# Performance work log

Measured on AMD Instinct MI355X. Metric: run time of the kernel, lower is better.

The kernel has to match this reference:

```python
import jax, jax.numpy as jnp
import numpy as np

B, S, D, H = 2, 2048, 1024, 16
DK = D // H

def setup_inputs() -> dict:
    key = jax.random.key(0)
    ks = jax.random.split(key, 12)
    s = 0.02
    inp = {
        'query': jax.random.normal(ks[0], (B, S, D), jnp.float32),
        'key':   jax.random.normal(ks[1], (B, S, D), jnp.float32),
        'value': jax.random.normal(ks[2], (B, S, D), jnp.float32),
        'mask':  jnp.broadcast_to(jnp.tril(jnp.ones((S, S), jnp.int32)), (B, S, S)),
        'wq': jax.random.normal(ks[3], (D, D), jnp.float32) * s,
        'bq': jnp.zeros((D,), jnp.float32),
        'wk': jax.random.normal(ks[4], (D, D), jnp.float32) * s,
        'bk': jnp.zeros((D,), jnp.float32),
        'wv': jax.random.normal(ks[5], (D, D), jnp.float32) * s,
        'bv': jnp.zeros((D,), jnp.float32),
        'wo': jax.random.normal(ks[6], (D, D), jnp.float32) * s,
        'bo': jnp.zeros((D,), jnp.float32),
    }
    return inp

def reference(query, key, value, mask, wq, bq, wk, bk, wv, bv, wo, bo):
    # Linear projections (torch Linear: x @ W.T + b); W stored (out,in)
    Q = query @ wq.T + bq   # (B,Sq,D)
    K = key   @ wk.T + bk   # (B,Sk,D)
    V = value @ wv.T + bv   # (B,Sk,D)
    # split heads -> (B,H,S,DK)
    Q = Q.reshape(B, S, H, DK).transpose(0, 2, 1, 3)
    K = K.reshape(B, S, H, DK).transpose(0, 2, 1, 3)
    V = V.reshape(B, S, H, DK).transpose(0, 2, 1, 3)
    scores = jnp.einsum('bhqd,bhkd->bhqk', Q, K) / jnp.sqrt(jnp.float32(DK))
    scores = jnp.where(mask[:, None, :, :] == 0, -jnp.inf, scores)
    attn = jax.nn.softmax(scores, axis=-1)  # dropout is identity in eval/reference
    context = jnp.einsum('bhqk,bhkd->bhqd', attn, V)
    context = context.transpose(0, 2, 1, 3).reshape(B, S, D)
    return context @ wo.T + bo
```

## Files before the change

### kernel.cpp

```cpp
#include <hip/hip_runtime.h>
#include <hip/hip_bf16.h>


#define B_ 2
#define S_ 2048
#define D_ 1024
#define H_ 16
#define DK_ 64
#define SZX (4096 * 1024)
#define SZW (1024 * 1024)

typedef __attribute__((ext_vector_type(8))) short short8;
typedef __attribute__((ext_vector_type(4))) float f32x4;
typedef __attribute__((ext_vector_type(16))) float f32x16;

using bf16 = __hip_bfloat16;

__device__ __forceinline__ short8 load8(const bf16* p) {
    return *reinterpret_cast<const short8*>(p);
}

__device__ __forceinline__ f32x4 mfma16(short8 a, short8 b, f32x4 c) {
    return __builtin_amdgcn_mfma_f32_16x16x32_bf16(a, b, c, 0, 0, 0);
}

__device__ __forceinline__ f32x16 mfma32(short8 a, short8 b, f32x16 c) {
    return __builtin_amdgcn_mfma_f32_32x32x16_bf16(a, b, c, 0, 0, 0);
}

__device__ __forceinline__ void async16(const bf16* g, bf16* l) {
    __builtin_amdgcn_global_load_lds(
        (const __attribute__((address_space(1))) void*)g,
        (__attribute__((address_space(3))) void*)l, 16, 0, 0);
}

__device__ __forceinline__ short bf16rne(float f) {
    unsigned u = __float_as_uint(f);
    return (short)((u + 0x7FFFu + ((u >> 16) & 1u)) >> 16);
}

struct CvtArgs {
    const float* src[7];
    bf16* dst[7];
};

__global__ __launch_bounds__(256) void cvt_kernel(CvtArgs a) {
    const long long e = ((long long)blockIdx.x * 256 + threadIdx.x) * 8;
    int t; long long off;
    if (e < 3LL * SZX) { t = (int)(e >> 22); off = e & (SZX - 1); }
    else { const long long e2 = e - 3LL * SZX; t = 3 + (int)(e2 >> 20); off = e2 & (SZW - 1); }
    const float4 f0 = *reinterpret_cast<const float4*>(a.src[t] + off);
    const float4 f1 = *reinterpret_cast<const float4*>(a.src[t] + off + 4);
    short8 o;
    o[0] = bf16rne(f0.x); o[1] = bf16rne(f0.y); o[2] = bf16rne(f0.z); o[3] = bf16rne(f0.w);
    o[4] = bf16rne(f1.x); o[5] = bf16rne(f1.y); o[6] = bf16rne(f1.z); o[7] = bf16rne(f1.w);
    *reinterpret_cast<short8*>((short*)a.dst[t] + off) = o;
}

struct ProjArgs {
    const bf16* X[3]; const bf16* W[3]; const float* bias[3]; void* Y[3]; int mode[3];
};

template <int BM>
__global__ __launch_bounds__(256) void proj_kernel(ProjArgs a) {
    constexpr int MSUB = BM / 32;
    constexpr int WM   = MSUB / 2;

    const int z = blockIdx.z;
    const bf16* __restrict__ X = a.X[z];
    const bf16* __restrict__ W = a.W[z];
    const float* __restrict__ bias = a.bias[z];
    const int mode = a.mode[z];

    __shared__ __align__(16) bf16 lA[MSUB * 4 * 512];
    __shared__ __align__(16) bf16 lB[16 * 512];

    const int tid  = threadIdx.x;
    const int wv   = tid >> 6;
    const int lane = tid & 63;
    const int l31  = lane & 31;
    const int khi  = lane >> 5;
    const int m0   = blockIdx.x * BM;
    const int n0   = blockIdx.y * 128;

    const bf16* gA[MSUB];
    #pragma unroll
    for (int s = 0; s < MSUB; ++s) {
        const int fa = wv * MSUB + s;
        gA[s] = X + (size_t)(m0 + (fa >> 2) * 32 + l31) * D_ + (fa & 3) * 16 + khi * 8;
    }
    const bf16* gB = W + (size_t)(n0 + wv * 32 + l31) * D_ + khi * 8;

    f32x16 acc[WM][2] = {};

    #pragma unroll 1
    for (int k0 = 0; k0 < D_; k0 += 64) {
        #pragma unroll
        for (int s = 0; s < MSUB; ++s)
            async16(gA[s] + k0, &lA[(wv * MSUB + s) * 512]);
        #pragma unroll
        for (int s = 0; s < 4; ++s)
            async16(gB + k0 + s * 16, &lB[(wv * 4 + s) * 512]);
        __syncthreads();

        #pragma unroll
        for (int kk = 0; kk < 4; ++kk) {
            short8 af[WM], bfr[2];
            #pragma unroll
            for (int mi = 0; mi < WM; ++mi)
                af[mi] = load8(&lA[(((wv & 1) * WM + mi) * 4 + kk) * 512 + lane * 8]);
            #pragma unroll
            for (int ni = 0; ni < 2; ++ni)
                bfr[ni] = load8(&lB[(((wv >> 1) * 2 + ni) * 4 + kk) * 512 + lane * 8]);
            #pragma unroll
            for (int mi = 0; mi < WM; ++mi)
                #pragma unroll
                for (int ni = 0; ni < 2; ++ni)
                    acc[mi][ni] = mfma32(af[mi], bfr[ni], acc[mi][ni]);
        }
        __syncthreads();
    }

    #pragma unroll
    for (int ni = 0; ni < 2; ++ni) {
        const int col = n0 + (wv >> 1) * 64 + ni * 32 + l31;
        const float bv = bias[col];
        const int h = col >> 6, d = col & 63;
        #pragma unroll
        for (int mi = 0; mi < WM; ++mi) {
            const int rb = m0 + ((wv & 1) * WM + mi) * 32 + 4 * khi;
            #pragma unroll
            for (int reg = 0; reg < 16; ++reg) {
                const int m = rb + (reg & 3) + 8 * (reg >> 2);
                const float val = acc[mi][ni][reg] + bv;
                if (mode == 3) {
                    ((float*)a.Y[z])[(size_t)m * D_ + col] = val;
                } else {
                    bf16* Y = (bf16*)a.Y[z];
                    const bf16 o = __float2bfloat16(val);
                    const int b  = m >> 11;
                    const int s  = m & (S_ - 1);
                    const int bh = b * H_ + h;
                    if (mode == 2) Y[((size_t)bh * DK_ + d) * S_ + s] = o;
                    else           Y[((size_t)bh * S_ + s) * DK_ + d] = o;
                }
            }
        }
    }
}

__global__ __launch_bounds__(256) void attn_kernel(
    const bf16* __restrict__ Qb, const bf16* __restrict__ Kb,
    const bf16* __restrict__ Vt, bf16* __restrict__ ctx)
{
    __shared__ __align__(16) bf16 Kt[64 * 64];
    __shared__ __align__(16) bf16 Vl[64 * 64];
    __shared__ __align__(16) bf16 lds_p[4][16][72];

    const int tid  = threadIdx.x;
    const int wv   = tid >> 6;
    const int lane = tid & 63;
    const int quad = lane >> 4;
    const int l16  = lane & 15;

    const int bx = blockIdx.x;
    const int bh = (bx & 7) * 4 + ((bx >> 3) & 3);
    const int m  = 31 - (bx >> 5);
    const int q0 = m * 64;
    const int qr = q0 + wv * 16;

    const bf16* Qh = Qb + (size_t)bh * (S_ * DK_);
    const bf16* Kh = Kb + (size_t)bh * (S_ * DK_);
    const bf16* Vh = Vt + (size_t)bh * (DK_ * S_);

    const float c = 0.18033688011112042f;
    const short8 ones = {16256, 16256, 16256, 16256, 16256, 16256, 16256, 16256};

    const int srow  = wv * 8 + (lane >> 3);
    const int sunit = (lane & 7) ^ ((lane >> 3) & 7);

    const short8 qa0 = load8(Qh + (qr + l16) * DK_ + quad * 8);
    const short8 qa1 = load8(Qh + (qr + l16) * DK_ + 32 + quad * 8);

    f32x4 cacc[4] = {};
    f32x4 lsum = {};

    for (int jt = 0; jt <= m; ++jt) {
        const int j0 = jt * 64;

        #pragma unroll
        for (int cc = 0; cc < 2; ++cc) {
            const int r = cc * 32 + srow;
            async16(Kh + (size_t)(j0 + r) * DK_ + sunit * 8, &Kt[(cc * 32 + wv * 8) * 64]);
            async16(Vh + (size_t)r * S_ + j0 + sunit * 8,    &Vl[(cc * 32 + wv * 8) * 64]);
        }
        __syncthreads();

        short8 kb[4][2], vb[4][2];
        #pragma unroll
        for (int t = 0; t < 4; ++t)
            #pragma unroll
            for (int kh = 0; kh < 2; ++kh) {
                const int u = ((kh * 4 + quad) ^ (l16 & 7)) * 8;
                kb[t][kh] = load8(&Kt[(t * 16 + l16) * 64 + u]);
                vb[t][kh] = load8(&Vl[(t * 16 + l16) * 64 + u]);
            }

        f32x4 s[4];
        #pragma unroll
        for (int t = 0; t < 4; ++t) {
            f32x4 zz = {};
            zz = mfma16(qa0, kb[t][0], zz);
            s[t] = mfma16(qa1, kb[t][1], zz);
        }

        if (jt < m) {
            #pragma unroll
            for (int r = 0; r < 4; ++r)
                #pragma unroll
                for (int t = 0; t < 4; ++t)
                    lds_p[wv][quad * 4 + r][t * 16 + l16] =
                        __float2bfloat16(exp2f(c * s[t][r]));
        } else {
            #pragma unroll
            for (int r = 0; r < 4; ++r) {
                const int row = qr + quad * 4 + r;
                #pragma unroll
                for (int t = 0; t < 4; ++t) {
                    const float p = (j0 + t * 16 + l16 <= row) ? exp2f(c * s[t][r]) : 0.f;
                    lds_p[wv][quad * 4 + r][t * 16 + l16] = __float2bfloat16(p);
                }
            }
        }

        asm volatile("s_waitcnt lgkmcnt(0)" ::: "memory");
        const short8 pa0 = load8(&lds_p[wv][l16][quad * 8]);
        const short8 pa1 = load8(&lds_p[wv][l16][32 + quad * 8]);

        #pragma unroll
        for (int dt = 0; dt < 4; ++dt) {
            cacc[dt] = mfma16(pa0, vb[dt][0], cacc[dt]);
            cacc[dt] = mfma16(pa1, vb[dt][1], cacc[dt]);
        }
        lsum = mfma16(pa0, ones, lsum);
        lsum = mfma16(pa1, ones, lsum);

        __syncthreads();
    }

    const int bb = bh >> 4, hh = bh & 15;
    #pragma unroll
    for (int r = 0; r < 4; ++r) {
        const float inv = 1.0f / lsum[r];
        const int row = qr + quad * 4 + r;
        bf16* orow = ctx + (size_t)(bb * S_ + row) * D_ + hh * DK_;
        #pragma unroll
        for (int dt = 0; dt < 4; ++dt)
            orow[dt * 16 + l16] = __float2bfloat16(cacc[dt][r] * inv);
    }
}

extern "C" void kernel_launch(void* const* d_in, const int* in_sizes, int n_in,
                              void* d_out, int out_size, void* d_ws, size_t ws_size,
                              hipStream_t stream) {
    (void)in_sizes; (void)n_in; (void)out_size; (void)ws_size;
    const float* q  = (const float*)d_in[0];
    const float* k  = (const float*)d_in[1];
    const float* v  = (const float*)d_in[2];
    const float* wq = (const float*)d_in[4];
    const float* bq = (const float*)d_in[5];
    const float* wk = (const float*)d_in[6];
    const float* bk = (const float*)d_in[7];
    const float* wv = (const float*)d_in[8];
    const float* bv = (const float*)d_in[9];
    const float* wo = (const float*)d_in[10];
    const float* bo = (const float*)d_in[11];

    bf16* base = (bf16*)d_ws;
    bf16* Qb  = base;
    bf16* Kb  = base + 1 * (size_t)SZX;
    bf16* Vt  = base + 2 * (size_t)SZX;
    bf16* ctx = base + 3 * (size_t)SZX;
    bf16* xq  = base + 4 * (size_t)SZX;
    bf16* xk  = base + 5 * (size_t)SZX;
    bf16* xv  = base + 6 * (size_t)SZX;
    bf16* wqb = base + 7 * (size_t)SZX;
    bf16* wkb = wqb + 1 * (size_t)SZW;
    bf16* wvb = wqb + 2 * (size_t)SZW;
    bf16* wob = wqb + 3 * (size_t)SZW;

    CvtArgs ca;
    ca.src[0] = q;  ca.src[1] = k;  ca.src[2] = v;
    ca.src[3] = wq; ca.src[4] = wk; ca.src[5] = wv; ca.src[6] = wo;
    ca.dst[0] = xq;  ca.dst[1] = xk;  ca.dst[2] = xv;
    ca.dst[3] = wqb; ca.dst[4] = wkb; ca.dst[5] = wvb; ca.dst[6] = wob;
    cvt_kernel<<<8192, 256, 0, stream>>>(ca);

    ProjArgs pa;
    pa.X[0] = xq;  pa.X[1] = xk;  pa.X[2] = xv;
    pa.W[0] = wqb; pa.W[1] = wkb; pa.W[2] = wvb;
    pa.bias[0] = bq; pa.bias[1] = bk; pa.bias[2] = bv;
    pa.Y[0] = Qb; pa.Y[1] = Kb; pa.Y[2] = Vt;
    pa.mode[0] = 0; pa.mode[1] = 1; pa.mode[2] = 2;
    proj_kernel<128><<<dim3(32, 8, 3), 256, 0, stream>>>(pa);

    attn_kernel<<<dim3(1024), 256, 0, stream>>>(Qb, Kb, Vt, ctx);

    ProjArgs po;
    po.X[0] = ctx; po.W[0] = wob; po.bias[0] = bo; po.Y[0] = d_out; po.mode[0] = 3;
    po.X[1] = ctx; po.W[1] = wob; po.bias[1] = bo; po.Y[1] = d_out; po.mode[1] = 3;
    po.X[2] = ctx; po.W[2] = wob; po.bias[2] = bo; po.Y[2] = d_out; po.mode[2] = 3;
    proj_kernel<64><<<dim3(64, 8, 1), 256, 0, stream>>>(po);
}
```

Before: 278.5 us.

## Use row-major XOR-swizzled LDS tiles and templated BN in projection GEMM

Rewrites the projection kernel's shared-memory staging. Each async 16-byte load now copies a contiguous 128-byte row chunk, and an XOR swizzle on the 16-byte unit index is meant to avoid LDS bank conflicts on the fragment reads. The kernel is templated on BN, and both projection launches drop from 128 to 64 output columns per block, which doubles the grid. More blocks improves occupancy and wave fill on the many CUs, at the cost of less reuse of each A tile per block.

```diff
diff --git a/kernel.cpp b/kernel.cpp
--- a/kernel.cpp
+++ b/kernel.cpp
@@ -61,10 +61,10 @@
     const bf16* X[3]; const bf16* W[3]; const float* bias[3]; void* Y[3]; int mode[3];
 };
 
-template <int BM>
+template <int BM, int BN>
 __global__ __launch_bounds__(256) void proj_kernel(ProjArgs a) {
-    constexpr int MSUB = BM / 32;
-    constexpr int WM   = MSUB / 2;
+    constexpr int WTM = BM / 2, WTN = BN / 2;
+    constexpr int WM = WTM / 32, WN = WTN / 32;
 
     const int z = blockIdx.z;
     const bf16* __restrict__ X = a.X[z];
@@ -72,63 +72,62 @@
     const float* __restrict__ bias = a.bias[z];
     const int mode = a.mode[z];
 
-    __shared__ __align__(16) bf16 lA[MSUB * 4 * 512];
-    __shared__ __align__(16) bf16 lB[16 * 512];
+    __shared__ __align__(16) bf16 lA[BM * 64];
+    __shared__ __align__(16) bf16 lB[BN * 64];
 
     const int tid  = threadIdx.x;
     const int wv   = tid >> 6;
     const int lane = tid & 63;
     const int l31  = lane & 31;
     const int khi  = lane >> 5;
+    const int r7   = l31 & 7;
     const int m0   = blockIdx.x * BM;
-    const int n0   = blockIdx.y * 128;
-
-    const bf16* gA[MSUB];
-    #pragma unroll
-    for (int s = 0; s < MSUB; ++s) {
-        const int fa = wv * MSUB + s;
-        gA[s] = X + (size_t)(m0 + (fa >> 2) * 32 + l31) * D_ + (fa & 3) * 16 + khi * 8;
-    }
-    const bf16* gB = W + (size_t)(n0 + wv * 32 + l31) * D_ + khi * 8;
-
-    f32x16 acc[WM][2] = {};
+    const int n0   = blockIdx.y * BN;
+
+    const int srow  = lane >> 3;
+    const int sunit = (lane & 7) ^ (srow & 7);
+    const bf16* gA = X + (size_t)(m0 + wv * (BM / 4) + srow) * D_ + sunit * 8;
+    const bf16* gB = W + (size_t)(n0 + wv * (BN / 4) + srow) * D_ + sunit * 8;
+
+    f32x16 acc[WM][WN] = {};
 
     #pragma unroll 1
     for (int k0 = 0; k0 < D_; k0 += 64) {
         #pragma unroll
-        for (int s = 0; s < MSUB; ++s)
-            async16(gA[s] + k0, &lA[(wv * MSUB + s) * 512]);
-        #pragma unroll
-        for (int s = 0; s < 4; ++s)
-            async16(gB + k0 + s * 16, &lB[(wv * 4 + s) * 512]);
+        for (int cc = 0; cc < BM / 32; ++cc)
+            async16(gA + (size_t)cc * 8 * D_ + k0, &lA[(wv * (BM / 4) + cc * 8) * 64]);
+        #pragma unroll
+        for (int cc = 0; cc < BN / 32; ++cc)
+            async16(gB + (size_t)cc * 8 * D_ + k0, &lB[(wv * (BN / 4) + cc * 8) * 64]);
         __syncthreads();
 
         #pragma unroll
         for (int kk = 0; kk < 4; ++kk) {
-            short8 af[WM], bfr[2];
+            const int up = ((kk * 2 + khi) ^ r7) * 8;
+            short8 af[WM], bfr[WN];
             #pragma unroll
             for (int mi = 0; mi < WM; ++mi)
-                af[mi] = load8(&lA[(((wv & 1) * WM + mi) * 4 + kk) * 512 + lane * 8]);
-            #pragma unroll
-            for (int ni = 0; ni < 2; ++ni)
-                bfr[ni] = load8(&lB[(((wv >> 1) * 2 + ni) * 4 + kk) * 512 + lane * 8]);
+                af[mi] = load8(&lA[((wv & 1) * WTM + mi * 32 + l31) * 64 + up]);
+            #pragma unroll
+            for (int ni = 0; ni < WN; ++ni)
+                bfr[ni] = load8(&lB[((wv >> 1) * WTN + ni * 32 + l31) * 64 + up]);
             #pragma unroll
             for (int mi = 0; mi < WM; ++mi)
                 #pragma unroll
-                for (int ni = 0; ni < 2; ++ni)
+                for (int ni = 0; ni < WN; ++ni)
                     acc[mi][ni] = mfma32(af[mi], bfr[ni], acc[mi][ni]);
         }
         __syncthreads();
     }
 
     #pragma unroll
-    for (int ni = 0; ni < 2; ++ni) {
-        const int col = n0 + (wv >> 1) * 64 + ni * 32 + l31;
+    for (int ni = 0; ni < WN; ++ni) {
+        const int col = n0 + (wv >> 1) * WTN + ni * 32 + l31;
         const float bv = bias[col];
         const int h = col >> 6, d = col & 63;
         #pragma unroll
         for (int mi = 0; mi < WM; ++mi) {
-            const int rb = m0 + ((wv & 1) * WM + mi) * 32 + 4 * khi;
+            const int rb = m0 + (wv & 1) * WTM + mi * 32 + 4 * khi;
             #pragma unroll
             for (int reg = 0; reg < 16; ++reg) {
                 const int m = rb + (reg & 3) + 8 * (reg >> 2);
@@ -302,7 +301,7 @@
     pa.bias[0] = bq; pa.bias[1] = bk; pa.bias[2] = bv;
     pa.Y[0] = Qb; pa.Y[1] = Kb; pa.Y[2] = Vt;
     pa.mode[0] = 0; pa.mode[1] = 1; pa.mode[2] = 2;
-    proj_kernel<128><<<dim3(32, 8, 3), 256, 0, stream>>>(pa);
+    proj_kernel<128, 64><<<dim3(32, 16, 3), 256, 0, stream>>>(pa);
 
     attn_kernel<<<dim3(1024), 256, 0, stream>>>(Qb, Kb, Vt, ctx);
 
@@ -310,5 +309,5 @@
     po.X[0] = ctx; po.W[0] = wob; po.bias[0] = bo; po.Y[0] = d_out; po.mode[0] = 3;
     po.X[1] = ctx; po.W[1] = wob; po.bias[1] = bo; po.Y[1] = d_out; po.mode[1] = 3;
     po.X[2] = ctx; po.W[2] = wob; po.bias[2] = bo; po.Y[2] = d_out; po.mode[2] = 3;
-    proj_kernel<64><<<dim3(64, 8, 1), 256, 0, stream>>>(po);
-}
+    proj_kernel<64, 64><<<dim3(64, 16, 1), 256, 0, stream>>>(po);
+}
```

New measurement: 248.3 us. -10.8%, faster.
